# Optimization experiments

Measured on AMD Instinct MI355X. Metric: run time of the kernel, lower is better.

The kernel has to match this reference:

```python
import jax, jax.numpy as jnp
import numpy as np

NUM_MAIN_SEQ_ATOMS = 12   # backbone atoms per RNA residue
NUM_NEIGHBOUR = 30
EMBEDDING_DIM = 32
EPS = 1e-5
BIG_DIST = 1000000.0


def setup_inputs() -> dict:
    key = jax.random.key(0)
    k1, k2, k3 = jax.random.split(key, 3)
    B, L, A = 2, 256, NUM_MAIN_SEQ_ATOMS
    coords = jax.random.normal(k1, (B, L, A, 3), dtype=jnp.float32) * 10.0
    mask = jax.random.randint(k2, (B, L), 0, 2).astype(jnp.int32)
    emb_table = jax.random.normal(k3, (NUM_MAIN_SEQ_ATOMS, EMBEDDING_DIM), dtype=jnp.float32)
    scale = jnp.ones((1, 1, EMBEDDING_DIM), dtype=jnp.float32)
    shift = jnp.zeros((1, 1, EMBEDDING_DIM), dtype=jnp.float32)
    return {"coords": coords, "mask": mask, "emb_table": emb_table,
            "scale": scale, "shift": shift}


def _graph_norm(features, m, scale, shift):
    # features: (B,N,E); m: (B,N) float {0,1}
    mm = m[:, :, None]                                   # (B,N,1)
    masked = features * mm
    cnt = jnp.maximum(mm.sum(axis=1, keepdims=True), 1.0)  # (B,1,1)
    mean = masked.sum(axis=1, keepdims=True) / cnt
    var = ((masked - mean) ** 2).sum(axis=1, keepdims=True) / cnt
    std = jnp.sqrt(var + EPS)
    out = ((features - mean) / std) * scale + shift
    return out * mm


def reference(coords, mask, emb_table, scale, shift):
    B, L, A, _ = coords.shape
    N = L * A
    atom_coords = coords.reshape(B, N, 3)
    atom_mask = jnp.repeat(mask, A, axis=1)              # (B,N) int
    m = atom_mask.astype(coords.dtype)

    # ---- encoder: cyclic atom-type embedding + graph norm ----
    atom_types = jnp.arange(N) % A                       # (N,)
    emb = emb_table[atom_types][None] * m[:, :, None]    # (B,N,E)
    encode = _graph_norm(emb, m, scale, shift)

    # ---- kNN graph: O(N^2) pairwise distances + masked top-k ----
    d = atom_coords[:, None, :, :] - atom_coords[:, :, None, :]  # (B,N,N,3)
    dist = jnp.sqrt((d ** 2).sum(-1) + 1e-6)             # (B,N,N)
    m2 = m[:, None, :] * m[:, :, None]                   # (B,N,N)
    dist = dist * m2 + (1.0 - m2) * BIG_DIST

    k = min(NUM_NEIGHBOUR, N)
    neg_d, edge_idx = jax.lax.top_k(-dist, k)            # smallest-k
    dist_neighbors = -neg_d                              # (B,N,k)

    pad = (atom_mask == 0)[:, :, None]                   # (B,N,1)
    edge_idx = jnp.where(pad, 0, edge_idx)
    dist_neighbors = jnp.where(pad, BIG_DIST, dist_neighbors)
    return atom_coords, atom_mask, encode, dist_neighbors, edge_idx
```

## Files before the change

kernel.cpp:

```cpp
#include <hip/hip_runtime.h>
#include <math.h>

#define NA   12
#define NL   256
#define NN   3072
#define NB   2
#define ED   32
#define KNB  30
#define BIGD 1000000.0f

#define OFF_COORDS 0
#define OFF_MASK   18432
#define OFF_ENC    24576
#define OFF_DIST   221184
#define OFF_IDX    405504

#define KEYVAL 0xFFFFF000u
#define KEYIDX 0x00000FFFu
#define MASKED_ADD 1e12f
#define VALID_ADD  1e-6f

static __device__ __forceinline__ unsigned umin32(unsigned a, unsigned b) {
    return a < b ? a : b;
}

#define DPP_MIN_STEP(CTRL)                                                        \
    {                                                                             \
        int t_ = __builtin_amdgcn_update_dpp(v_, v_, (CTRL), 0xf, 0xf, false);    \
        v_ = (int)umin32((unsigned)v_, (unsigned)t_);                             \
    }

#define TREE8(A0,A1,A2,A3,A4,A5,A6,A7) \
    umin32(umin32(umin32((A0),(A1)), umin32((A2),(A3))), \
           umin32(umin32((A4),(A5)), umin32((A6),(A7))))

#define REMOVE_RESCAN(G)                                                          \
    {                                                                             \
        _Pragma("unroll")                                                         \
        for (int u = 0; u < 8; ++u) {                                             \
            const int t = (G) * 8 + u;                                            \
            k[t] = (k[t] == wkey) ? 0xFFFFFFFFu : k[t];                           \
        }                                                                         \
        gm[(G)] = TREE8(k[(G)*8+0],k[(G)*8+1],k[(G)*8+2],k[(G)*8+3],              \
                        k[(G)*8+4],k[(G)*8+5],k[(G)*8+6],k[(G)*8+7]);             \
    }

__global__ __launch_bounds__(256, 3) void fused_kernel(const float* __restrict__ coords,
                                                       const int* __restrict__ mask,
                                                       const float* __restrict__ emb,
                                                       const float* __restrict__ scale,
                                                       const float* __restrict__ shift,
                                                       float* __restrict__ out) {
    __shared__ float4 sc4[NN];

    int tid  = threadIdx.x;
    int lane = tid & 63;
    int wave = tid >> 6;
    int b    = (int)(blockIdx.x) / 384;
    int rblk = (int)(blockIdx.x) - b * 384;
    const float* cb = coords + (size_t)b * NN * 3;
    const int*   mb = mask + b * NL;

#pragma unroll
    for (int s = 0; s < 12; ++s) {
        int e = tid + s * 256;
        int r = (e * 43691) >> 19;
        float aw = mb[r] ? VALID_ADD : MASKED_ADD;
        sc4[e] = make_float4(cb[3 * e + 0], cb[3 * e + 1], cb[3 * e + 2], aw);
    }
    __syncthreads();

#pragma unroll 1
    for (int rr = 0; rr < 2; ++rr) {
        int i   = rblk * 8 + wave * 2 + rr;
        int row = b * NN + i;
        float4 q = sc4[i];

        if (q.w < 1.0f) {
            unsigned k[48];
            unsigned gm[6];

#pragma unroll
            for (int t = 0; t < 48; ++t) {
                int j = t * 64 + lane;
                float4 v = sc4[j];
                float dx = v.x - q.x, dy = v.y - q.y, dz = v.z - q.z;
                float s = fmaf(dx, dx, fmaf(dy, dy, fmaf(dz, dz, v.w)));
                k[t] = (__float_as_uint(s) & KEYVAL) | (unsigned)j;
            }
#pragma unroll
            for (int g = 0; g < 6; ++g)
                gm[g] = TREE8(k[g*8+0],k[g*8+1],k[g*8+2],k[g*8+3],
                              k[g*8+4],k[g*8+5],k[g*8+6],k[g*8+7]);

            unsigned cur = umin32(umin32(umin32(gm[0], gm[1]), umin32(gm[2], gm[3])),
                                  umin32(gm[4], gm[5]));
            unsigned rkey = 0u;

            for (int it = 0; it < KNB; ++it) {
                int v_ = (int)cur;
                DPP_MIN_STEP(0xB1)
                DPP_MIN_STEP(0x4E)
                DPP_MIN_STEP(0x141)
                DPP_MIN_STEP(0x140)
                unsigned r0  = (unsigned)__builtin_amdgcn_readlane(v_, 0);
                unsigned r16 = (unsigned)__builtin_amdgcn_readlane(v_, 16);
                unsigned r32 = (unsigned)__builtin_amdgcn_readlane(v_, 32);
                unsigned r48 = (unsigned)__builtin_amdgcn_readlane(v_, 48);
                unsigned wkey = umin32(umin32(r0, r16), umin32(r32, r48));
                rkey = (lane == it) ? wkey : rkey;

                int wg = (int)((wkey & KEYIDX) >> 9);
                switch (wg) {
                    case 0: REMOVE_RESCAN(0); break;
                    case 1: REMOVE_RESCAN(1); break;
                    case 2: REMOVE_RESCAN(2); break;
                    case 3: REMOVE_RESCAN(3); break;
                    case 4: REMOVE_RESCAN(4); break;
                    default: REMOVE_RESCAN(5); break;
                }
                cur = umin32(umin32(umin32(gm[0], gm[1]), umin32(gm[2], gm[3])),
                             umin32(gm[4], gm[5]));
            }

            if (lane < KNB) {
                float d2 = __uint_as_float(rkey & KEYVAL);
                out[OFF_DIST + (size_t)row * KNB + lane] = sqrtf(d2);
                out[OFF_IDX  + (size_t)row * KNB + lane] = (float)(rkey & KEYIDX);
            }
        } else {
            if (lane < KNB) {
                out[OFF_DIST + (size_t)row * KNB + lane] = BIGD;
                out[OFF_IDX  + (size_t)row * KNB + lane] = 0.f;
            }
        }
    }

    int gidx = (int)blockIdx.x * 256 + tid;

    {
        const int4* m4 = (const int4*)(mask + b * NL);
        int4 mv = m4[lane];
        float S = (float)(mv.x + mv.y + mv.z + mv.w);
#pragma unroll
        for (int m = 1; m < 64; m <<= 1) S += __shfl_xor(S, m);

        int c = gidx & (ED - 1);
        float colsum = 0.f, sumsq = 0.f;
#pragma unroll
        for (int a = 0; a < NA; ++a) {
            float e = emb[a * ED + c];
            colsum += e; sumsq += e * e;
        }
        float cnt  = fmaxf(12.0f * S, 1.0f);
        float mean = S * colsum / cnt;
        float acc  = sumsq - 2.0f * mean * colsum + 12.0f * mean * mean;
        float var  = (S * acc + ((float)NN - 12.0f * S) * mean * mean) / cnt;
        float rstd = 1.0f / sqrtf(var + 1e-5f);

        int n  = (gidx >> 5) - b * NN;
        int nr = (n * 43691) >> 19;
        float v = 0.f;
        if (sc4[n].w < 1.0f) {
            float en = emb[(n - nr * NA) * ED + c];
            v = (en - mean) * rstd * scale[c] + shift[c];
        }
        out[OFF_ENC + gidx] = v;
    }

    if (gidx < NB * NN * 3) {
        out[OFF_COORDS + gidx] = coords[gidx];
    }

    if (gidx < NB * NN) {
        int bb = gidx >= NN ? 1 : 0;
        int nn = gidx - bb * NN;
        int nr = (nn * 43691) >> 19;
        out[OFF_MASK + gidx] = (float)mask[bb * NL + nr];
    }
}

extern "C" void kernel_launch(void* const* d_in, const int* in_sizes, int n_in,
                              void* d_out, int out_size, void* d_ws, size_t ws_size,
                              hipStream_t stream) {
    const float* coords = (const float*)d_in[0];
    const int*   mask   = (const int*)d_in[1];
    const float* emb    = (const float*)d_in[2];
    const float* scale  = (const float*)d_in[3];
    const float* shift  = (const float*)d_in[4];
    float* out = (float*)d_out;

    fused_kernel<<<NB * (NN / 8), 256, 0, stream>>>(coords, mask, emb, scale, shift, out);
}
```

Before: 93.84 us.

## Drop shared-memory coordinate staging and split top-k and prep into separate blocks

The kernel no longer stages the 3072 coordinates of a batch into LDS. Each wave now handles one query row and reads candidate coordinates and mask straight from global memory through the cache. The encoder, coords copy and mask copy move to a separate group of blocks in the same launch. This removes the per-block LDS fill and barrier, frees LDS so more waves can be resident, and lets masked rows exit early. The cost is strided 3-float global loads with repeated mask lookups in the inner loop, which may be slower than LDS reads.

```diff
diff --git a/kernel.cpp b/kernel.cpp
--- a/kernel.cpp
+++ b/kernel.cpp
@@ -19,6 +19,9 @@
 #define KEYIDX 0x00000FFFu
 #define MASKED_ADD 1e12f
 #define VALID_ADD  1e-6f
+
+#define NTOPK_BLK 1536
+#define NPREP_BLK 768
 
 static __device__ __forceinline__ unsigned umin32(unsigned a, unsigned b) {
     return a < b ? a : b;
@@ -45,100 +48,91 @@
                         k[(G)*8+4],k[(G)*8+5],k[(G)*8+6],k[(G)*8+7]);             \
     }
 
-__global__ __launch_bounds__(256, 3) void fused_kernel(const float* __restrict__ coords,
-                                                       const int* __restrict__ mask,
-                                                       const float* __restrict__ emb,
-                                                       const float* __restrict__ scale,
-                                                       const float* __restrict__ shift,
-                                                       float* __restrict__ out) {
-    __shared__ float4 sc4[NN];
+__global__ __launch_bounds__(256, 2) void fat_kernel(const float* __restrict__ coords,
+                                                     const int* __restrict__ mask,
+                                                     const float* __restrict__ emb,
+                                                     const float* __restrict__ scale,
+                                                     const float* __restrict__ shift,
+                                                     float* __restrict__ out) {
+    int tid = threadIdx.x;
+    int bid = (int)blockIdx.x;
 
-    int tid  = threadIdx.x;
-    int lane = tid & 63;
-    int wave = tid >> 6;
-    int b    = (int)(blockIdx.x) / 384;
-    int rblk = (int)(blockIdx.x) - b * 384;
-    const float* cb = coords + (size_t)b * NN * 3;
-    const int*   mb = mask + b * NL;
+    if (bid < NTOPK_BLK) {
+        int lane = tid & 63;
+        int row  = bid * 4 + (tid >> 6);
+        int b = (row >= NN) ? 1 : 0;
+        int i = row - b * NN;
+        const float* cb = coords + (size_t)b * NN * 3;
+        const int*   mb = mask + b * NL;
 
-#pragma unroll
-    for (int s = 0; s < 12; ++s) {
-        int e = tid + s * 256;
-        int r = (e * 43691) >> 19;
-        float aw = mb[r] ? VALID_ADD : MASKED_ADD;
-        sc4[e] = make_float4(cb[3 * e + 0], cb[3 * e + 1], cb[3 * e + 2], aw);
-    }
-    __syncthreads();
-
-#pragma unroll 1
-    for (int rr = 0; rr < 2; ++rr) {
-        int i   = rblk * 8 + wave * 2 + rr;
-        int row = b * NN + i;
-        float4 q = sc4[i];
-
-        if (q.w < 1.0f) {
-            unsigned k[48];
-            unsigned gm[6];
-
-#pragma unroll
-            for (int t = 0; t < 48; ++t) {
-                int j = t * 64 + lane;
-                float4 v = sc4[j];
-                float dx = v.x - q.x, dy = v.y - q.y, dz = v.z - q.z;
-                float s = fmaf(dx, dx, fmaf(dy, dy, fmaf(dz, dz, v.w)));
-                k[t] = (__float_as_uint(s) & KEYVAL) | (unsigned)j;
-            }
-#pragma unroll
-            for (int g = 0; g < 6; ++g)
-                gm[g] = TREE8(k[g*8+0],k[g*8+1],k[g*8+2],k[g*8+3],
-                              k[g*8+4],k[g*8+5],k[g*8+6],k[g*8+7]);
-
-            unsigned cur = umin32(umin32(umin32(gm[0], gm[1]), umin32(gm[2], gm[3])),
-                                  umin32(gm[4], gm[5]));
-            unsigned rkey = 0u;
-
-            for (int it = 0; it < KNB; ++it) {
-                int v_ = (int)cur;
-                DPP_MIN_STEP(0xB1)
-                DPP_MIN_STEP(0x4E)
-                DPP_MIN_STEP(0x141)
-                DPP_MIN_STEP(0x140)
-                unsigned r0  = (unsigned)__builtin_amdgcn_readlane(v_, 0);
-                unsigned r16 = (unsigned)__builtin_amdgcn_readlane(v_, 16);
-                unsigned r32 = (unsigned)__builtin_amdgcn_readlane(v_, 32);
-                unsigned r48 = (unsigned)__builtin_amdgcn_readlane(v_, 48);
-                unsigned wkey = umin32(umin32(r0, r16), umin32(r32, r48));
-                rkey = (lane == it) ? wkey : rkey;
-
-                int wg = (int)((wkey & KEYIDX) >> 9);
-                switch (wg) {
-                    case 0: REMOVE_RESCAN(0); break;
-                    case 1: REMOVE_RESCAN(1); break;
-                    case 2: REMOVE_RESCAN(2); break;
-                    case 3: REMOVE_RESCAN(3); break;
-                    case 4: REMOVE_RESCAN(4); break;
-                    default: REMOVE_RESCAN(5); break;
-                }
-                cur = umin32(umin32(umin32(gm[0], gm[1]), umin32(gm[2], gm[3])),
-                             umin32(gm[4], gm[5]));
-            }
-
-            if (lane < KNB) {
-                float d2 = __uint_as_float(rkey & KEYVAL);
-                out[OFF_DIST + (size_t)row * KNB + lane] = sqrtf(d2);
-                out[OFF_IDX  + (size_t)row * KNB + lane] = (float)(rkey & KEYIDX);
-            }
-        } else {
+        int qvalid = mb[(i * 43691) >> 19];
+        if (!qvalid) {
             if (lane < KNB) {
                 out[OFF_DIST + (size_t)row * KNB + lane] = BIGD;
                 out[OFF_IDX  + (size_t)row * KNB + lane] = 0.f;
             }
+            return;
         }
-    }
+        float qx = cb[i * 3 + 0], qy = cb[i * 3 + 1], qz = cb[i * 3 + 2];
 
-    int gidx = (int)blockIdx.x * 256 + tid;
+        unsigned k[48];
+        unsigned gm[6];
 
-    {
+#pragma unroll
+        for (int t = 0; t < 48; ++t) {
+            int j = t * 64 + lane;
+            int r = (j * 43691) >> 19;
+            float w = mb[r] ? VALID_ADD : MASKED_ADD;
+            float x = cb[j * 3 + 0], y = cb[j * 3 + 1], z = cb[j * 3 + 2];
+            float dx = x - qx, dy = y - qy, dz = z - qz;
+            float s = fmaf(dx, dx, fmaf(dy, dy, fmaf(dz, dz, w)));
+            k[t] = (__float_as_uint(s) & KEYVAL) | (unsigned)j;
+        }
+#pragma unroll
+        for (int g = 0; g < 6; ++g)
+            gm[g] = TREE8(k[g*8+0],k[g*8+1],k[g*8+2],k[g*8+3],
+                          k[g*8+4],k[g*8+5],k[g*8+6],k[g*8+7]);
+
+        unsigned cur = umin32(umin32(umin32(gm[0], gm[1]), gm[2]),
+                              umin32(umin32(gm[3], gm[4]), gm[5]));
+        unsigned rkey = 0u;
+
+        for (int it = 0; it < KNB; ++it) {
+            int v_ = (int)cur;
+            DPP_MIN_STEP(0xB1)
+            DPP_MIN_STEP(0x4E)
+            DPP_MIN_STEP(0x141)
+            DPP_MIN_STEP(0x140)
+            unsigned r0  = (unsigned)__builtin_amdgcn_readlane(v_, 0);
+            unsigned r16 = (unsigned)__builtin_amdgcn_readlane(v_, 16);
+            unsigned r32 = (unsigned)__builtin_amdgcn_readlane(v_, 32);
+            unsigned r48 = (unsigned)__builtin_amdgcn_readlane(v_, 48);
+            unsigned wkey = umin32(umin32(r0, r16), umin32(r32, r48));
+            rkey = (lane == it) ? wkey : rkey;
+
+            int wg = (int)((wkey & KEYIDX) >> 9);
+            switch (wg) {
+                case 0: REMOVE_RESCAN(0); break;
+                case 1: REMOVE_RESCAN(1); break;
+                case 2: REMOVE_RESCAN(2); break;
+                case 3: REMOVE_RESCAN(3); break;
+                case 4: REMOVE_RESCAN(4); break;
+                default: REMOVE_RESCAN(5); break;
+            }
+            cur = umin32(umin32(umin32(gm[0], gm[1]), gm[2]),
+                         umin32(umin32(gm[3], gm[4]), gm[5]));
+        }
+
+        if (lane < KNB) {
+            float d2 = __uint_as_float(rkey & KEYVAL);
+            out[OFF_DIST + (size_t)row * KNB + lane] = sqrtf(d2);
+            out[OFF_IDX  + (size_t)row * KNB + lane] = (float)(rkey & KEYIDX);
+        }
+    } else {
+        int gidx = (bid - NTOPK_BLK) * 256 + tid;
+        int lane = tid & 63;
+        int b = gidx / (NN * ED);
+
         const int4* m4 = (const int4*)(mask + b * NL);
         int4 mv = m4[lane];
         float S = (float)(mv.x + mv.y + mv.z + mv.w);
@@ -158,25 +152,25 @@
         float var  = (S * acc + ((float)NN - 12.0f * S) * mean * mean) / cnt;
         float rstd = 1.0f / sqrtf(var + 1e-5f);
 
-        int n  = (gidx >> 5) - b * NN;
+        int n  = (gidx >> 5) % NN;
         int nr = (n * 43691) >> 19;
+        int mi = mask[b * NL + nr];
         float v = 0.f;
-        if (sc4[n].w < 1.0f) {
+        if (mi) {
             float en = emb[(n - nr * NA) * ED + c];
             v = (en - mean) * rstd * scale[c] + shift[c];
         }
         out[OFF_ENC + gidx] = v;
-    }
 
-    if (gidx < NB * NN * 3) {
-        out[OFF_COORDS + gidx] = coords[gidx];
-    }
-
-    if (gidx < NB * NN) {
-        int bb = gidx >= NN ? 1 : 0;
-        int nn = gidx - bb * NN;
-        int nr = (nn * 43691) >> 19;
-        out[OFF_MASK + gidx] = (float)mask[bb * NL + nr];
+        if (gidx < NB * NN * 3) {
+            out[OFF_COORDS + gidx] = coords[gidx];
+        }
+        if (gidx < NB * NN) {
+            int bb = gidx >= NN ? 1 : 0;
+            int nn = gidx - bb * NN;
+            int rr = (nn * 43691) >> 19;
+            out[OFF_MASK + gidx] = (float)mask[bb * NL + rr];
+        }
     }
 }
 
@@ -190,5 +184,6 @@
     const float* shift  = (const float*)d_in[4];
     float* out = (float*)d_out;
 
-    fused_kernel<<<NB * (NN / 8), 256, 0, stream>>>(coords, mask, emb, scale, shift, out);
+    fat_kernel<<<NTOPK_BLK + NPREP_BLK, 256, 0, stream>>>(
+        coords, mask, emb, scale, shift, out);
 }
```

After: 86.52 us. -7.8%, faster.
